# Optimization experiments

Measured on AMD Instinct MI355X. Metric: run time of the kernel, lower is better.

## Reference

```python
import jax, jax.numpy as jnp
import numpy as np

D_IN = 1024
D_OUT = 1024
N_HEADS = 16
HEAD_DIM = D_OUT // N_HEADS


def setup_inputs() -> dict:
    key = jax.random.key(0)
    ks = jax.random.split(key, 5)
    scale = 0.02
    x = jax.random.normal(ks[0], (2, 2048, D_IN), dtype=jnp.float32)
    Wq = jax.random.normal(ks[1], (D_IN, D_OUT), dtype=jnp.float32) * scale
    Wk = jax.random.normal(ks[2], (D_IN, D_OUT), dtype=jnp.float32) * scale
    Wv = jax.random.normal(ks[3], (D_IN, D_OUT), dtype=jnp.float32) * scale
    Wout = jax.random.normal(ks[4], (D_OUT, D_OUT), dtype=jnp.float32) * scale
    return {"x": x, "Wq": Wq, "Wk": Wk, "Wv": Wv, "Wout": Wout}


def reference(x, Wq, Wk, Wv, Wout):
    batch, seq_len, _ = x.shape
    # projections (no bias)
    Q = (x @ Wq).reshape(batch, seq_len, N_HEADS, HEAD_DIM)
    K = (x @ Wk).reshape(batch, seq_len, N_HEADS, HEAD_DIM)
    V = (x @ Wv).reshape(batch, seq_len, N_HEADS, HEAD_DIM)
    # scores: [batch, heads, seq, seq]
    scores = jnp.einsum("bqhd,bkhd->bhqk", Q, K) / jnp.sqrt(
        jnp.asarray(HEAD_DIM, dtype=x.dtype)
    )
    # causal mask: positions k > q masked to -inf
    causal = jnp.tril(jnp.ones((seq_len, seq_len), dtype=bool))
    scores = jnp.where(causal[None, None], scores, -jnp.inf)
    weights = jax.nn.softmax(scores, axis=-1)
    vectors = jnp.einsum("bhqk,bkhd->bqhd", weights, V)
    vectors = vectors.reshape(batch, seq_len, D_OUT)
    return vectors @ Wout
```

## Files before the change

kernel.cpp:

```cpp
#include <hip/hip_runtime.h>
#include <hip/hip_bf16.h>


typedef __attribute__((ext_vector_type(8))) _Float16 vhalf8;
typedef __attribute__((ext_vector_type(4))) _Float16 vhalf4;
typedef __attribute__((ext_vector_type(4))) float vfloat4;

#define D_MODEL 1024
#define SEQ     2048
#define NB      2
#define NH      16
#define HD      64

#define SCALE_K1 0.18033688f
#define SCALE_K2 (-5.77078016f)

__device__ __forceinline__ void async16(const void* g, void* l) {
  __builtin_amdgcn_global_load_lds(
      (const __attribute__((address_space(1))) unsigned int*)g,
      (__attribute__((address_space(3))) unsigned int*)l, 16, 0, 0);
}

__global__ __launch_bounds__(256) void cvt_f32_f16(
    const float* __restrict__ in, _Float16* __restrict__ out) {
  size_t i = ((size_t)blockIdx.x * 256 + threadIdx.x) * 8;
  float4 a = *(const float4*)&in[i];
  float4 b = *(const float4*)&in[i + 4];
  vhalf8 h;
  h[0] = (_Float16)a.x; h[1] = (_Float16)a.y;
  h[2] = (_Float16)a.z; h[3] = (_Float16)a.w;
  h[4] = (_Float16)b.x; h[5] = (_Float16)b.y;
  h[6] = (_Float16)b.z; h[7] = (_Float16)b.w;
  *(vhalf8*)&out[i] = h;
}

__global__ __launch_bounds__(256) void transpose_w(
    const float* __restrict__ in, _Float16* __restrict__ out, int R, int C) {
  __shared__ _Float16 tile[64][65];
  int c0 = blockIdx.x * 64, r0 = blockIdx.y * 64;
  int t = threadIdx.x;
  int tc = t & 63, tr = t >> 6;
#pragma unroll
  for (int p = 0; p < 16; p++) {
    int r = tr + p * 4;
    tile[r][tc] = (_Float16)in[(size_t)(r0 + r) * C + c0 + tc];
  }
  __syncthreads();
#pragma unroll
  for (int p = 0; p < 16; p++) {
    int r = tr + p * 4;
    out[(size_t)(c0 + r) * R + r0 + tc] = tile[tc][r];
  }
}

__global__ __launch_bounds__(256) void transpose_v(
    const _Float16* __restrict__ QKV, _Float16* __restrict__ Vt) {
  __shared__ _Float16 tile[64][65];
  int bh = blockIdx.y;
  int b = bh >> 4, h = bh & 15;
  int s0 = blockIdx.x * 64;
  int t = threadIdx.x;
  int tc = t & 63, tr = t >> 6;
#pragma unroll
  for (int p = 0; p < 16; p++) {
    int s = tr + p * 4;
    tile[s][tc] = QKV[(size_t)(b * SEQ + s0 + s) * 3072 + 2048 + h * HD + tc];
  }
  __syncthreads();
#pragma unroll
  for (int p = 0; p < 16; p++) {
    int d = tr + p * 4;
    Vt[((size_t)bh * HD + d) * SEQ + s0 + tc] = tile[tc][d];
  }
}

__global__ __launch_bounds__(256) void gemm128(
    const _Float16* __restrict__ A, const _Float16* __restrict__ Bt,
    _Float16* __restrict__ Ch, float* __restrict__ Cf,
    int M, int N, int K, int write_f32) {
  __shared__ _Float16 As[128 * 32];
  __shared__ _Float16 Bs[128 * 32];
  int m0 = blockIdx.x * 128, n0 = blockIdx.y * 128;
  int t = threadIdx.x;
  int lane = t & 63, wave = t >> 6;
  int wm = (wave >> 1) * 64, wn = (wave & 1) * 64;
  int col = lane & 15, quad = lane >> 4;

  int srow = lane >> 2;
  int skc = (lane & 3) << 3;

  vfloat4 acc[4][4];
#pragma unroll
  for (int i = 0; i < 4; i++)
#pragma unroll
    for (int j = 0; j < 4; j++) {
      acc[i][j][0] = 0.f; acc[i][j][1] = 0.f;
      acc[i][j][2] = 0.f; acc[i][j][3] = 0.f;
    }

  for (int k0 = 0; k0 < K; k0 += 32) {
    __syncthreads();
#pragma unroll
    for (int j = 0; j < 4; j++) {
      int c = wave * 4 + j;
      int row = ((c & 7) << 4) + srow;
      if (c < 8)
        async16(&A[(size_t)(m0 + row) * K + k0 + skc], &As[c * 512]);
      else
        async16(&Bt[(size_t)(n0 + row) * K + k0 + skc], &Bs[(c - 8) * 512]);
    }
    __syncthreads();

    vhalf8 af[4], bf[4];
#pragma unroll
    for (int i = 0; i < 4; i++) {
      af[i] = *(const vhalf8*)&As[(wm + i * 16 + col) * 32 + quad * 8];
      bf[i] = *(const vhalf8*)&Bs[(wn + i * 16 + col) * 32 + quad * 8];
    }
#pragma unroll
    for (int i = 0; i < 4; i++)
#pragma unroll
      for (int j = 0; j < 4; j++)
        acc[i][j] = __builtin_amdgcn_mfma_f32_16x16x32_f16(af[i], bf[j], acc[i][j], 0, 0, 0);
  }

#pragma unroll
  for (int i = 0; i < 4; i++)
#pragma unroll
    for (int j = 0; j < 4; j++)
#pragma unroll
      for (int r = 0; r < 4; r++) {
        int m = m0 + wm + i * 16 + quad * 4 + r;
        int n = n0 + wn + j * 16 + col;
        if (write_f32)
          Cf[(size_t)m * N + n] = acc[i][j][r];
        else
          Ch[(size_t)m * N + n] = (_Float16)acc[i][j][r];
      }
}

__global__ __launch_bounds__(256) void attn(
    const _Float16* __restrict__ QKV, const _Float16* __restrict__ Vt,
    _Float16* __restrict__ Vec) {
  int blk = blockIdx.x;
  int j = blk >> 5;
  int hb = blk & 31;
  int k8 = j >> 3, jp = j & 7;
  int qt = (k8 & 1) ? (8 * k8 + 7 - jp) : (8 * k8 + jp);
  int h = hb & 15;
  int b = hb >> 4;
  int q0 = qt * 64;

  const _Float16* Qb  = QKV + (size_t)(b * SEQ) * 3072 + h * HD;
  const _Float16* Kb  = QKV + (size_t)(b * SEQ) * 3072 + 1024 + h * HD;
  const _Float16* Vtb = Vt + (size_t)(b * NH + h) * HD * SEQ;

  int t = threadIdx.x;
  int lane = t & 63, wave = t >> 6;
  int col = lane & 15, quad = lane >> 4;
  int wq0 = q0 + wave * 16;

  __shared__ _Float16 Ks[64][72];
  __shared__ _Float16 Vs[64][72];
  __shared__ _Float16 Ps[4][16][72];

  vhalf8 qf0 = *(const vhalf8*)&Qb[(size_t)(wq0 + col) * 3072 + quad * 8];
  vhalf8 qf1 = *(const vhalf8*)&Qb[(size_t)(wq0 + col) * 3072 + 32 + quad * 8];

  vfloat4 o[4];
#pragma unroll
  for (int i = 0; i < 4; i++) { o[i][0]=0.f; o[i][1]=0.f; o[i][2]=0.f; o[i][3]=0.f; }
  float lsum[4] = {0.f, 0.f, 0.f, 0.f};

  int srow = t >> 2;
  int scol = (t & 3) * 16;
  int kslot = ((srow & 3) << 4) + (srow >> 2);

  for (int kb = 0; kb <= q0 + 63; kb += 64) {
    __syncthreads();
    {
      const _Float16* kg = &Kb[(size_t)(kb + srow) * 3072 + scol];
      *(vhalf8*)&Ks[kslot][scol]     = *(const vhalf8*)kg;
      *(vhalf8*)&Ks[kslot][scol + 8] = *(const vhalf8*)(kg + 8);
      const _Float16* vg = &Vtb[(size_t)srow * SEQ + kb + scol];
      *(vhalf8*)&Vs[srow][scol]     = *(const vhalf8*)vg;
      *(vhalf8*)&Vs[srow][scol + 8] = *(const vhalf8*)(vg + 8);
    }
    __syncthreads();

    if (kb <= wq0 + 15) {
      vfloat4 s[4];
#pragma unroll
      for (int hh = 0; hh < 4; hh++) {
        vhalf8 kf0 = *(const vhalf8*)&Ks[hh * 16 + col][quad * 8];
        vhalf8 kf1 = *(const vhalf8*)&Ks[hh * 16 + col][32 + quad * 8];
        vfloat4 z; z[0]=0.f; z[1]=0.f; z[2]=0.f; z[3]=0.f;
        z = __builtin_amdgcn_mfma_f32_16x16x32_f16(qf0, kf0, z, 0, 0, 0);
        z = __builtin_amdgcn_mfma_f32_16x16x32_f16(qf1, kf1, z, 0, 0, 0);
        s[hh] = z;
      }
      bool diag = (kb + 63 > wq0);
#pragma unroll
      for (int r = 0; r < 4; r++) {
        int q = wq0 + quad * 4 + r;
        float p[4];
#pragma unroll
        for (int hh = 0; hh < 4; hh++) {
          float sc = fmaf(s[hh][r], SCALE_K1, SCALE_K2);
          if (diag && (kb + 4 * col + hh > q)) sc = -1e30f;
          p[hh] = __builtin_exp2f(sc);
        }
        lsum[r] += (p[0] + p[1]) + (p[2] + p[3]);
        vhalf4 ph;
        ph[0] = (_Float16)p[0]; ph[1] = (_Float16)p[1];
        ph[2] = (_Float16)p[2]; ph[3] = (_Float16)p[3];
        *(vhalf4*)&Ps[wave][quad * 4 + r][4 * col] = ph;
      }
      __asm__ __volatile__("s_waitcnt lgkmcnt(0)" ::: "memory");
      vhalf8 pf0 = *(const vhalf8*)&Ps[wave][col][quad * 8];
      vhalf8 pf1 = *(const vhalf8*)&Ps[wave][col][32 + quad * 8];
#pragma unroll
      for (int tt = 0; tt < 4; tt++) {
        vhalf8 vf0 = *(const vhalf8*)&Vs[tt * 16 + col][quad * 8];
        vhalf8 vf1 = *(const vhalf8*)&Vs[tt * 16 + col][32 + quad * 8];
        o[tt] = __builtin_amdgcn_mfma_f32_16x16x32_f16(pf0, vf0, o[tt], 0, 0, 0);
        o[tt] = __builtin_amdgcn_mfma_f32_16x16x32_f16(pf1, vf1, o[tt], 0, 0, 0);
      }
    }
  }

  float inv_l[4];
#pragma unroll
  for (int r = 0; r < 4; r++) {
    float rs = lsum[r];
#pragma unroll
    for (int msk = 1; msk < 16; msk <<= 1) rs += __shfl_xor(rs, msk, 64);
    inv_l[r] = 1.0f / rs;
  }
#pragma unroll
  for (int tt = 0; tt < 4; tt++)
#pragma unroll
    for (int r = 0; r < 4; r++) {
      int q = wq0 + quad * 4 + r;
      int d = tt * 16 + col;
      Vec[(size_t)(b * SEQ + q) * D_MODEL + h * HD + d] =
          (_Float16)(o[tt][r] * inv_l[r]);
    }
}

extern "C" void kernel_launch(void* const* d_in, const int* in_sizes, int n_in,
                              void* d_out, int out_size, void* d_ws, size_t ws_size,
                              hipStream_t stream) {
  const float* x  = (const float*)d_in[0];
  const float* Wq = (const float*)d_in[1];
  const float* Wk = (const float*)d_in[2];
  const float* Wv = (const float*)d_in[3];
  const float* Wo = (const float*)d_in[4];
  float* out = (float*)d_out;

  char* ws = (char*)d_ws;
  _Float16* Xh     = (_Float16*)ws;
  _Float16* Wt_qkv = (_Float16*)(ws + 8388608);
  _Float16* Wot    = (_Float16*)(ws + 14680064);
  _Float16* QKV    = (_Float16*)(ws + 16777216);
  _Float16* Vt     = (_Float16*)(ws + 41943040);
  _Float16* Vec    = (_Float16*)(ws + 50331648);

  dim3 tb(256);
  cvt_f32_f16<<<dim3(2048), tb, 0, stream>>>(x, Xh);
  transpose_w<<<dim3(16, 16), tb, 0, stream>>>(Wq, Wt_qkv, 1024, 1024);
  transpose_w<<<dim3(16, 16), tb, 0, stream>>>(Wk, Wt_qkv + 1024 * 1024, 1024, 1024);
  transpose_w<<<dim3(16, 16), tb, 0, stream>>>(Wv, Wt_qkv + 2 * 1024 * 1024, 1024, 1024);
  transpose_w<<<dim3(16, 16), tb, 0, stream>>>(Wo, Wot, 1024, 1024);

  gemm128<<<dim3(32, 24), tb, 0, stream>>>(Xh, Wt_qkv, QKV, nullptr, 4096, 3072, 1024, 0);
  transpose_v<<<dim3(32, 32), tb, 0, stream>>>(QKV, Vt);
  attn<<<dim3(NB * NH * (SEQ / 64)), tb, 0, stream>>>(QKV, Vt, Vec);
  gemm128<<<dim3(32, 8), tb, 0, stream>>>(Vec, Wot, nullptr, out, 4096, 1024, 1024, 1);
}
```

Baseline: 208.2 us.

## Fuse V transpose into QKV GEMM, merge weight transposes, prefetch K/V in attention

Merges the four weight-transpose launches into one 3D-grid kernel. The QKV GEMM epilogue now writes the V columns directly in transposed layout, which removes the separate transpose_v pass. The attention kernel pre-scales Q in fp16 so the per-score FMA disappears, prefetches the next K/V tile into registers while the current one is being computed, and switches to a plain reverse-order tile schedule. Risks are strided scattered stores in the GEMM epilogue for the V part, possible fp16 overflow in exp2 because the max-shift constant is gone, and extra register pressure from the prefetch.

New measurement: 193.4 us. -7.1%, faster.

```diff
diff --git a/kernel.cpp b/kernel.cpp
--- a/kernel.cpp
+++ b/kernel.cpp
@@ -13,7 +13,6 @@
 #define HD      64
 
 #define SCALE_K1 0.18033688f
-#define SCALE_K2 (-5.77078016f)
 
 __device__ __forceinline__ void async16(const void* g, void* l) {
   __builtin_amdgcn_global_load_lds(
@@ -34,50 +33,34 @@
   *(vhalf8*)&out[i] = h;
 }
 
-__global__ __launch_bounds__(256) void transpose_w(
-    const float* __restrict__ in, _Float16* __restrict__ out, int R, int C) {
+__global__ __launch_bounds__(256) void transpose_w4(
+    const float* __restrict__ Wq, const float* __restrict__ Wk,
+    const float* __restrict__ Wv, const float* __restrict__ Wo,
+    _Float16* __restrict__ Wt_qkv, _Float16* __restrict__ Wot) {
   __shared__ _Float16 tile[64][65];
+  int z = blockIdx.z;
+  const float* in = (z == 0) ? Wq : (z == 1) ? Wk : (z == 2) ? Wv : Wo;
+  _Float16* out = (z < 3) ? (Wt_qkv + (size_t)z * 1024 * 1024) : Wot;
   int c0 = blockIdx.x * 64, r0 = blockIdx.y * 64;
   int t = threadIdx.x;
   int tc = t & 63, tr = t >> 6;
 #pragma unroll
   for (int p = 0; p < 16; p++) {
     int r = tr + p * 4;
-    tile[r][tc] = (_Float16)in[(size_t)(r0 + r) * C + c0 + tc];
+    tile[r][tc] = (_Float16)in[(size_t)(r0 + r) * 1024 + c0 + tc];
   }
   __syncthreads();
 #pragma unroll
   for (int p = 0; p < 16; p++) {
     int r = tr + p * 4;
-    out[(size_t)(c0 + r) * R + r0 + tc] = tile[tc][r];
-  }
-}
-
-__global__ __launch_bounds__(256) void transpose_v(
-    const _Float16* __restrict__ QKV, _Float16* __restrict__ Vt) {
-  __shared__ _Float16 tile[64][65];
-  int bh = blockIdx.y;
-  int b = bh >> 4, h = bh & 15;
-  int s0 = blockIdx.x * 64;
-  int t = threadIdx.x;
-  int tc = t & 63, tr = t >> 6;
-#pragma unroll
-  for (int p = 0; p < 16; p++) {
-    int s = tr + p * 4;
-    tile[s][tc] = QKV[(size_t)(b * SEQ + s0 + s) * 3072 + 2048 + h * HD + tc];
-  }
-  __syncthreads();
-#pragma unroll
-  for (int p = 0; p < 16; p++) {
-    int d = tr + p * 4;
-    Vt[((size_t)bh * HD + d) * SEQ + s0 + tc] = tile[tc][d];
+    out[(size_t)(c0 + r) * 1024 + r0 + tc] = tile[tc][r];
   }
 }
 
 __global__ __launch_bounds__(256) void gemm128(
     const _Float16* __restrict__ A, const _Float16* __restrict__ Bt,
     _Float16* __restrict__ Ch, float* __restrict__ Cf,
-    int M, int N, int K, int write_f32) {
+    _Float16* __restrict__ Vt, int M, int N, int K, int mode) {
   __shared__ _Float16 As[128 * 32];
   __shared__ _Float16 Bs[128 * 32];
   int m0 = blockIdx.x * 128, n0 = blockIdx.y * 128;
@@ -85,7 +68,6 @@
   int lane = t & 63, wave = t >> 6;
   int wm = (wave >> 1) * 64, wn = (wave & 1) * 64;
   int col = lane & 15, quad = lane >> 4;
-
   int srow = lane >> 2;
   int skc = (lane & 3) << 3;
 
@@ -124,6 +106,7 @@
         acc[i][j] = __builtin_amdgcn_mfma_f32_16x16x32_f16(af[i], bf[j], acc[i][j], 0, 0, 0);
   }
 
+  bool vmode = (mode == 2) && (n0 >= 2048);
 #pragma unroll
   for (int i = 0; i < 4; i++)
 #pragma unroll
@@ -132,10 +115,16 @@
       for (int r = 0; r < 4; r++) {
         int m = m0 + wm + i * 16 + quad * 4 + r;
         int n = n0 + wn + j * 16 + col;
-        if (write_f32)
+        if (mode == 1) {
           Cf[(size_t)m * N + n] = acc[i][j][r];
-        else
+        } else if (vmode) {
+          int nn = n - 2048;
+          int hh = nn >> 6, dd = nn & 63;
+          int bb = m >> 11, ss = m & 2047;
+          Vt[(((size_t)bb * NH + hh) * HD + dd) * SEQ + ss] = (_Float16)acc[i][j][r];
+        } else {
           Ch[(size_t)m * N + n] = (_Float16)acc[i][j][r];
+        }
       }
 }
 
@@ -143,10 +132,8 @@
     const _Float16* __restrict__ QKV, const _Float16* __restrict__ Vt,
     _Float16* __restrict__ Vec) {
   int blk = blockIdx.x;
-  int j = blk >> 5;
+  int qt = 31 - (blk >> 5);
   int hb = blk & 31;
-  int k8 = j >> 3, jp = j & 7;
-  int qt = (k8 & 1) ? (8 * k8 + 7 - jp) : (8 * k8 + jp);
   int h = hb & 15;
   int b = hb >> 4;
   int q0 = qt * 64;
@@ -166,6 +153,11 @@
 
   vhalf8 qf0 = *(const vhalf8*)&Qb[(size_t)(wq0 + col) * 3072 + quad * 8];
   vhalf8 qf1 = *(const vhalf8*)&Qb[(size_t)(wq0 + col) * 3072 + 32 + quad * 8];
+#pragma unroll
+  for (int i = 0; i < 8; i++) {
+    qf0[i] = qf0[i] * (_Float16)SCALE_K1;
+    qf1[i] = qf1[i] * (_Float16)SCALE_K1;
+  }
 
   vfloat4 o[4];
 #pragma unroll
@@ -176,17 +168,27 @@
   int scol = (t & 3) * 16;
   int kslot = ((srow & 3) << 4) + (srow >> 2);
 
+  vhalf8 kr0, kr1, vr0, vr1;
+  {
+    const _Float16* kg = &Kb[(size_t)srow * 3072 + scol];
+    kr0 = *(const vhalf8*)kg; kr1 = *(const vhalf8*)(kg + 8);
+    const _Float16* vg = &Vtb[(size_t)srow * SEQ + scol];
+    vr0 = *(const vhalf8*)vg; vr1 = *(const vhalf8*)(vg + 8);
+  }
+
   for (int kb = 0; kb <= q0 + 63; kb += 64) {
-    __syncthreads();
-    {
-      const _Float16* kg = &Kb[(size_t)(kb + srow) * 3072 + scol];
-      *(vhalf8*)&Ks[kslot][scol]     = *(const vhalf8*)kg;
-      *(vhalf8*)&Ks[kslot][scol + 8] = *(const vhalf8*)(kg + 8);
-      const _Float16* vg = &Vtb[(size_t)srow * SEQ + kb + scol];
-      *(vhalf8*)&Vs[srow][scol]     = *(const vhalf8*)vg;
-      *(vhalf8*)&Vs[srow][scol + 8] = *(const vhalf8*)(vg + 8);
-    }
-    __syncthreads();
+    *(vhalf8*)&Ks[kslot][scol]     = kr0;
+    *(vhalf8*)&Ks[kslot][scol + 8] = kr1;
+    *(vhalf8*)&Vs[srow][scol]      = vr0;
+    *(vhalf8*)&Vs[srow][scol + 8]  = vr1;
+    __syncthreads();
+
+    if (kb < q0) {
+      const _Float16* kg = &Kb[(size_t)(kb + 64 + srow) * 3072 + scol];
+      kr0 = *(const vhalf8*)kg; kr1 = *(const vhalf8*)(kg + 8);
+      const _Float16* vg = &Vtb[(size_t)srow * SEQ + kb + 64 + scol];
+      vr0 = *(const vhalf8*)vg; vr1 = *(const vhalf8*)(vg + 8);
+    }
 
     if (kb <= wq0 + 15) {
       vfloat4 s[4];
@@ -206,7 +208,7 @@
         float p[4];
 #pragma unroll
         for (int hh = 0; hh < 4; hh++) {
-          float sc = fmaf(s[hh][r], SCALE_K1, SCALE_K2);
+          float sc = s[hh][r];
           if (diag && (kb + 4 * col + hh > q)) sc = -1e30f;
           p[hh] = __builtin_exp2f(sc);
         }
@@ -227,6 +229,7 @@
         o[tt] = __builtin_amdgcn_mfma_f32_16x16x32_f16(pf1, vf1, o[tt], 0, 0, 0);
       }
     }
+    __syncthreads();
   }
 
   float inv_l[4];
@@ -268,13 +271,11 @@
 
   dim3 tb(256);
   cvt_f32_f16<<<dim3(2048), tb, 0, stream>>>(x, Xh);
-  transpose_w<<<dim3(16, 16), tb, 0, stream>>>(Wq, Wt_qkv, 1024, 1024);
-  transpose_w<<<dim3(16, 16), tb, 0, stream>>>(Wk, Wt_qkv + 1024 * 1024, 1024, 1024);
-  transpose_w<<<dim3(16, 16), tb, 0, stream>>>(Wv, Wt_qkv + 2 * 1024 * 1024, 1024, 1024);
-  transpose_w<<<dim3(16, 16), tb, 0, stream>>>(Wo, Wot, 1024, 1024);
-
-  gemm128<<<dim3(32, 24), tb, 0, stream>>>(Xh, Wt_qkv, QKV, nullptr, 4096, 3072, 1024, 0);
-  transpose_v<<<dim3(32, 32), tb, 0, stream>>>(QKV, Vt);
+  transpose_w4<<<dim3(16, 16, 4), tb, 0, stream>>>(Wq, Wk, Wv, Wo, Wt_qkv, Wot);
+
+  gemm128<<<dim3(32, 24), tb, 0, stream>>>(Xh, Wt_qkv, QKV, nullptr, Vt,
+                                           4096, 3072, 1024, 2);
   attn<<<dim3(NB * NH * (SEQ / 64)), tb, 0, stream>>>(QKV, Vt, Vec);
-  gemm128<<<dim3(32, 8), tb, 0, stream>>>(Vec, Wot, nullptr, out, 4096, 1024, 1024, 1);
-}
+  gemm128<<<dim3(32, 8), tb, 0, stream>>>(Vec, Wot, nullptr, out, nullptr,
+                                          4096, 1024, 1024, 1);
+}
```
